# Performance work log

Hardware: AMD Instinct MI355X
Metric: run time of the kernel (lower is better)

The kernel has to match this reference:

```python
import jax, jax.numpy as jnp
import numpy as np

HID = 256   # hidden_dim
P = 16      # pool_size
EPS = 1e-5


def _ln(x, g, b):
    m = x.mean(-1, keepdims=True)
    v = x.var(-1, keepdims=True)
    return (x - m) * jax.lax.rsqrt(v + EPS) * g + b


def setup_inputs() -> dict:
    key = jax.random.key(0)
    ks = jax.random.split(key, 12)
    B, Cf, H, W = 8, 512, 64, 64
    Cg = Cf // 2
    Co = Cf // 2
    s = 0.02
    d = {}
    d['e_f'] = jax.random.normal(ks[0], (B, Cf, H, W), jnp.float32)
    d['e_g'] = jax.random.normal(ks[1], (B, Cg, H, W), jnp.float32)
    d['l_feat'] = jax.random.normal(ks[2], (B, 768, 20), jnp.float32)
    d['l_mask'] = jnp.ones((B, 20, 1), jnp.float32)
    d['ln_f_g'] = jnp.ones((Cf,), jnp.float32)
    d['ln_f_b'] = jnp.zeros((Cf,), jnp.float32)
    d['ln_g_g'] = jnp.ones((Cg,), jnp.float32)
    d['ln_g_b'] = jnp.zeros((Cg,), jnp.float32)
    d['wq'] = jax.random.normal(ks[3], (Cf, HID), jnp.float32) * s
    d['bq'] = jnp.zeros((HID,), jnp.float32)
    d['wk'] = jax.random.normal(ks[4], (Cg, HID), jnp.float32) * s
    d['bk'] = jnp.zeros((HID,), jnp.float32)
    d['wv'] = jax.random.normal(ks[5], (Cg, HID), jnp.float32) * s
    d['bv'] = jnp.zeros((HID,), jnp.float32)
    d['wo'] = jax.random.normal(ks[6], (HID, HID), jnp.float32) * s
    d['bo'] = jnp.zeros((HID,), jnp.float32)
    d['dw_k'] = jax.random.normal(ks[7], (HID, 1, 3, 3), jnp.float32) * s  # depthwise kernel (OIHW, I=1)
    d['efp_w'] = jax.random.normal(ks[8], (HID, Cf), jnp.float32) * s     # 1x1 conv v_channels->hidden
    d['efp_b'] = jnp.zeros((HID,), jnp.float32)
    d['outc_w'] = jax.random.normal(ks[9], (Co, HID), jnp.float32) * s    # 1x1 conv hidden->out
    d['outc_b'] = jnp.zeros((Co,), jnp.float32)
    d['bn_g'] = jnp.ones((Co,), jnp.float32)
    d['bn_b'] = jnp.zeros((Co,), jnp.float32)
    d['bn_m'] = jnp.zeros((Co,), jnp.float32)
    d['bn_v'] = jnp.ones((Co,), jnp.float32)
    return d


def reference(e_f, e_g, l_feat, l_mask, ln_f_g, ln_f_b, ln_g_g, ln_g_b,
              wq, bq, wk, bk, wv, bv, wo, bo, dw_k, efp_w, efp_b,
              outc_w, outc_b, bn_g, bn_b, bn_m, bn_v):
    B, Cf, H, W = e_f.shape
    # Q = w_qi(LN(e_f))                                  (B, HW, HID)
    q = _ln(e_f.transpose(0, 2, 3, 1), ln_f_g, ln_f_b).reshape(B, H * W, Cf) @ wq + bq
    # K/V projections from LN(e_g)
    g = _ln(e_g.transpose(0, 2, 3, 1), ln_g_g, ln_g_b).reshape(B, H * W, -1)
    k = (g @ wk + bk).reshape(B, H, W, HID)
    v = (g @ wv + bv).reshape(B, H, W, HID)
    # 16x16 max/avg pooling -> (B, Hp*Wp, HID)
    k = jnp.max(k.reshape(B, H // P, P, W // P, P, HID), axis=(2, 4)).reshape(B, -1, HID)
    v = jnp.mean(v.reshape(B, H // P, P, W // P, P, HID), axis=(2, 4)).reshape(B, -1, HID)
    # pooled attention
    attn = jax.nn.softmax(jnp.einsum('bqd,bkd->bqk', q, k) * (HID ** -0.5), axis=-1)
    a_i = jnp.einsum('bqk,bkd->bqd', attn, v)  # (B, HW, HID)
    # depthwise 3x3 conv on Q (NCHW)
    q_nchw = q.reshape(B, H, W, HID).transpose(0, 3, 1, 2)
    dw = jax.lax.conv_general_dilated(q_nchw, dw_k, (1, 1), [(1, 1), (1, 1)],
                                      feature_group_count=HID)
    combined = dw + a_i.reshape(B, H, W, HID).transpose(0, 3, 1, 2)
    comb = combined.transpose(0, 2, 3, 1).reshape(B, H * W, HID) @ wo + bo
    comb = comb.reshape(B, H, W, HID).transpose(0, 3, 1, 2)
    # 1x1 proj of e_f, elementwise gate
    efp = jnp.einsum('bchw,oc->bohw', e_f, efp_w) + efp_b[None, :, None, None]
    e_a = efp * comb
    # out: 1x1 conv + BN (inference) + ReLU (dropout inactive in eval)
    out = jnp.einsum('bchw,oc->bohw', e_a, outc_w) + outc_b[None, :, None, None]
    scale = (bn_g * jax.lax.rsqrt(bn_v + EPS))[None, :, None, None]
    out = (out - bn_m[None, :, None, None]) * scale + bn_b[None, :, None, None]
    return jax.nn.relu(out)
```

## Files before the change

kernel.cpp:

```cpp
#include <hip/hip_runtime.h>
#include <math.h>

#define EPS 1e-5f

typedef __attribute__((ext_vector_type(8))) short bf16x8;
typedef __attribute__((ext_vector_type(4))) float f32x4;

__device__ __forceinline__ unsigned short f2bf(float f) {
    unsigned int u = __float_as_uint(f);
    u += 0x7fff + ((u >> 16) & 1);
    return (unsigned short)(u >> 16);
}
__device__ __forceinline__ float bf2f(unsigned short h) {
    return __uint_as_float(((unsigned int)h) << 16);
}
__device__ __forceinline__ float lof(unsigned int u) {
    return __uint_as_float(u << 16);
}
__device__ __forceinline__ float hif(unsigned int u) {
    return __uint_as_float(u & 0xffff0000u);
}
__device__ __forceinline__ void async16(void* lds, const void* g) {
    __builtin_amdgcn_global_load_lds(
        (const __attribute__((address_space(1))) unsigned int*)g,
        (__attribute__((address_space(3))) unsigned int*)lds, 16, 0, 0);
}

__global__ __launch_bounds__(256) void prep_all(
    const float* __restrict__ lnfg, const float* __restrict__ lnfb,
    const float* __restrict__ wq, const float* __restrict__ bq,
    const float* __restrict__ efpw, const float* __restrict__ efpb,
    const float* __restrict__ lngg, const float* __restrict__ lngb,
    const float* __restrict__ wk, const float* __restrict__ bk,
    const float* __restrict__ wv, const float* __restrict__ bv,
    const float* __restrict__ wo, const float* __restrict__ outcw,
    const float* __restrict__ outcb, const float* __restrict__ bng,
    const float* __restrict__ bnb, const float* __restrict__ bnm,
    const float* __restrict__ bnv, const float* __restrict__ dwk,
    unsigned short* __restrict__ Wb1t, unsigned short* __restrict__ Wb2t,
    unsigned short* __restrict__ Wot, unsigned short* __restrict__ Woc,
    float* __restrict__ dwt,
    float* __restrict__ cs1, float* __restrict__ cst1,
    float* __restrict__ cs2, float* __restrict__ cst2,
    float* __restrict__ scv, float* __restrict__ shv)
{
    int idx = blockIdx.x * 256 + threadIdx.x;
    if (idx < 262144) {
        int n = idx >> 9, k = idx & 511;
        float v = (n < 256) ? lnfg[k] * wq[k * 256 + n]
                            : efpw[(size_t)(n - 256) * 512 + k];
        Wb1t[idx] = f2bf(v);
    } else if (idx < 327680) {
        int j = idx - 262144; int n = j >> 8, k = j & 255;
        Wb2t[j] = f2bf(lngg[k] * wk[k * 256 + n]);
    } else if (idx < 393216) {
        int j = idx - 327680; int n = j >> 8, k = j & 255;
        Wot[j] = f2bf(wo[k * 256 + n]);
    } else if (idx < 458752) {
        int j = idx - 393216;
        Woc[j] = f2bf(outcw[j]);
    } else if (idx < 461056) {
        int j = idx - 458752; int tap = j >> 8, ch = j & 255;
        dwt[j] = dwk[ch * 9 + tap];
    } else if (idx < 462336) {
        int j = idx - 461056;
        if (j < 256) {
            int n = j; float cs = 0.f, ct = 0.f;
            for (int k = 0; k < 512; k++) {
                float w = wq[k * 256 + n];
                cs += lnfg[k] * w; ct += lnfb[k] * w;
            }
            cs1[n] = cs; cst1[n] = ct + bq[n];
        } else if (j < 512) {
            cs1[j] = 0.f; cst1[j] = efpb[j - 256];
        } else if (j < 768) {
            int n = j - 512; float cs = 0.f, ct = 0.f;
            for (int k = 0; k < 256; k++) {
                float w = wk[k * 256 + n];
                cs += lngg[k] * w; ct += lngb[k] * w;
            }
            cs2[n] = cs; cst2[n] = ct + bk[n];
        } else if (j < 1024) {
            int n = j - 768; float cs = 0.f, ct = 0.f;
            for (int k = 0; k < 256; k++) {
                float w = wv[k * 256 + n];
                cs += lngg[k] * w; ct += lngb[k] * w;
            }
            cs2[256 + n] = cs; cst2[256 + n] = ct + bv[n];
        } else {
            int n = j - 1024;
            float s = bng[n] * rsqrtf(bnv[n] + EPS);
            scv[n] = s;
            shv[n] = (outcb[n] - bnm[n]) * s + bnb[n];
        }
    }
}

__global__ __launch_bounds__(256) void transpose_fg(
    const float* __restrict__ ef, const float* __restrict__ eg,
    unsigned short* __restrict__ ef_bf, unsigned short* __restrict__ eg_bf,
    float* __restrict__ pf, float* __restrict__ pfq,
    float* __restrict__ pg, float* __restrict__ pgq)
{
    __shared__ float tile[64][65];
    __shared__ float psum[4][64], pss[4][64];
    int id = blockIdx.x;
    const float* src; unsigned short* dst; float* ps; float* pq;
    int C, cblk, b, p0;
    if (id < 2048) {
        src = ef; dst = ef_bf; ps = pf; pq = pfq; C = 512;
        b = id >> 8; cblk = (id >> 5) & 7; p0 = (id & 31) * 128;
    } else {
        id -= 2048;
        src = eg; dst = eg_bf; ps = pg; pq = pgq; C = 256;
        b = id >> 7; cblk = (id >> 5) & 3; p0 = (id & 31) * 128;
    }
    int c0 = cblk * 64;
    const float* s = src + ((size_t)b * C + c0) * 4096 + p0;
    int t = threadIdx.x;
    int cr = t >> 4, p4 = (t & 15) * 4;
    int lane = t & 63, grp = t >> 6;
    int pr = t >> 3, c8 = (t & 7) * 8;

    float4 r1[4], r2[4];
#pragma unroll
    for (int i = 0; i < 4; i++)
        r1[i] = *(const float4*)(s + (size_t)(i * 16 + cr) * 4096 + p4);
#pragma unroll
    for (int i = 0; i < 4; i++)
        r2[i] = *(const float4*)(s + (size_t)(i * 16 + cr) * 4096 + 64 + p4);

#pragma unroll
    for (int half = 0; half < 2; half++) {
#pragma unroll
        for (int i = 0; i < 4; i++) {
            float4 v = half ? r2[i] : r1[i];
            int c = i * 16 + cr;
            tile[c][p4 + 0] = v.x; tile[c][p4 + 1] = v.y;
            tile[c][p4 + 2] = v.z; tile[c][p4 + 3] = v.w;
        }
        __syncthreads();

        int pbase = p0 + half * 64;
        unsigned short* d = dst + ((size_t)(b * 4096 + pbase)) * C + c0;
#pragma unroll
        for (int i = 0; i < 2; i++) {
            int p = i * 32 + pr;
            uint4 pk;
            pk.x = (unsigned)f2bf(tile[c8 + 0][p]) | ((unsigned)f2bf(tile[c8 + 1][p]) << 16);
            pk.y = (unsigned)f2bf(tile[c8 + 2][p]) | ((unsigned)f2bf(tile[c8 + 3][p]) << 16);
            pk.z = (unsigned)f2bf(tile[c8 + 4][p]) | ((unsigned)f2bf(tile[c8 + 5][p]) << 16);
            pk.w = (unsigned)f2bf(tile[c8 + 6][p]) | ((unsigned)f2bf(tile[c8 + 7][p]) << 16);
            *(uint4*)(d + (size_t)p * C + c8) = pk;
        }

        float sm = 0.f, sq = 0.f;
#pragma unroll
        for (int j = 0; j < 16; j++) {
            float v = tile[grp * 16 + j][lane];
            sm += v; sq += v * v;
        }
        psum[grp][lane] = sm; pss[grp][lane] = sq;
        __syncthreads();
        if (t < 64) {
            float fs = psum[0][t] + psum[1][t] + psum[2][t] + psum[3][t];
            float fq = pss[0][t] + pss[1][t] + pss[2][t] + pss[3][t];
            ps[cblk * 32768 + b * 4096 + pbase + t] = fs;
            pq[cblk * 32768 + b * 4096 + pbase + t] = fq;
        }
        if (half == 0) __syncthreads();
    }
}

__global__ __launch_bounds__(256) void ln_finalize(
    const float* __restrict__ pf, const float* __restrict__ pfq,
    const float* __restrict__ pg, const float* __restrict__ pgq,
    float* __restrict__ mf, float* __restrict__ rf,
    float* __restrict__ mg, float* __restrict__ rg)
{
    int gp = blockIdx.x * 256 + threadIdx.x;
    float s = 0.f, q = 0.f;
#pragma unroll
    for (int i = 0; i < 8; i++) { s += pf[i * 32768 + gp]; q += pfq[i * 32768 + gp]; }
    float m = s * (1.f / 512.f);
    float v = q * (1.f / 512.f) - m * m;
    mf[gp] = m; rf[gp] = rsqrtf(v + EPS);
    s = 0.f; q = 0.f;
#pragma unroll
    for (int i = 0; i < 4; i++) { s += pg[i * 32768 + gp]; q += pgq[i * 32768 + gp]; }
    m = s * (1.f / 256.f);
    v = q * (1.f / 256.f) - m * m;
    mg[gp] = m; rg[gp] = rsqrtf(v + EPS);
}

template<int K>
__device__ __forceinline__ void mfma_core(
    const unsigned short* __restrict__ A, const unsigned short* __restrict__ Bt,
    int m0, int n0, unsigned short* As, unsigned short* Bs, f32x4 acc[4][4])
{
    const int tid = threadIdx.x;
    const int wave = tid >> 6, lane = tid & 63;
    const int wm = (wave & 1) * 64, wn = (wave >> 1) * 64;
#pragma unroll
    for (int i = 0; i < 4; i++)
#pragma unroll
        for (int j = 0; j < 4; j++) acc[i][j] = (f32x4){0.f, 0.f, 0.f, 0.f};

    const int srow = wave * 32 + (lane >> 3);
    const int sg = (lane & 7) ^ ((lane >> 3) & 7);
    const unsigned short* ga = A + (size_t)(m0 + srow) * K + sg * 8;
    const unsigned short* gb = Bt + (size_t)(n0 + srow) * K + sg * 8;

    for (int k0 = 0; k0 < K; k0 += 64) {
#pragma unroll
        for (int t = 0; t < 4; t++) {
            async16(As + (wave * 32 + t * 8) * 64, ga + (size_t)t * 8 * K + k0);
            async16(Bs + (wave * 32 + t * 8) * 64, gb + (size_t)t * 8 * K + k0);
        }
        __syncthreads();
#pragma unroll
        for (int ks = 0; ks < 2; ks++) {
            bf16x8 af[4], bfr[4];
            int kb = ks * 4 + (lane >> 4);
            int slot = (kb ^ (lane & 7)) * 8;
#pragma unroll
            for (int i = 0; i < 4; i++) {
                int m = wm + i * 16 + (lane & 15);
                af[i] = *(const bf16x8*)&As[m * 64 + slot];
                int n = wn + i * 16 + (lane & 15);
                bfr[i] = *(const bf16x8*)&Bs[n * 64 + slot];
            }
#pragma unroll
            for (int i = 0; i < 4; i++)
#pragma unroll
                for (int j = 0; j < 4; j++)
                    acc[i][j] = __builtin_amdgcn_mfma_f32_16x16x32_bf16(
                        af[i], bfr[j], acc[i][j], 0, 0, 0);
        }
        __syncthreads();
    }
}

__global__ __launch_bounds__(256, 2) void gemm1_mfma(
    const unsigned short* __restrict__ ef_bf, const unsigned short* __restrict__ Wb1t,
    const float* __restrict__ cs1, const float* __restrict__ cst1,
    const float* __restrict__ mf, const float* __restrict__ rf,
    unsigned short* __restrict__ qbuf, unsigned short* __restrict__ efpbuf)
{
    __shared__ unsigned short As[128 * 64];
    __shared__ unsigned short Bs[256 * 64];
    f32x4 acc[4][8];
    const int tid = threadIdx.x;
    const int wave = tid >> 6, lane = tid & 63;
    const int wm = (wave & 1) * 64, wn = (wave >> 1) * 128;
    const int m0 = blockIdx.x * 128, n0 = blockIdx.y * 256;
#pragma unroll
    for (int i = 0; i < 4; i++)
#pragma unroll
        for (int j = 0; j < 8; j++) acc[i][j] = (f32x4){0.f, 0.f, 0.f, 0.f};

    const int srow = lane >> 3;
    const int sg = (lane & 7) ^ (srow & 7);
    const unsigned short* ga = ef_bf + (size_t)(m0 + wave * 32 + srow) * 512 + sg * 8;
    const unsigned short* gb = Wb1t + (size_t)(n0 + wave * 64 + srow) * 512 + sg * 8;

    for (int k0 = 0; k0 < 512; k0 += 64) {
#pragma unroll
        for (int t = 0; t < 4; t++)
            async16(As + (wave * 32 + t * 8) * 64, ga + (size_t)t * 8 * 512 + k0);
#pragma unroll
        for (int t = 0; t < 8; t++)
            async16(Bs + (wave * 64 + t * 8) * 64, gb + (size_t)t * 8 * 512 + k0);
        __syncthreads();
#pragma unroll
        for (int ks = 0; ks < 2; ks++) {
            bf16x8 af[4], bfr[8];
            int kb = ks * 4 + (lane >> 4);
            int slot = (kb ^ (lane & 7)) * 8;
#pragma unroll
            for (int i = 0; i < 4; i++)
                af[i] = *(const bf16x8*)&As[(wm + i * 16 + (lane & 15)) * 64 + slot];
#pragma unroll
            for (int j = 0; j < 8; j++)
                bfr[j] = *(const bf16x8*)&Bs[(wn + j * 16 + (lane & 15)) * 64 + slot];
#pragma unroll
            for (int i = 0; i < 4; i++)
#pragma unroll
                for (int j = 0; j < 8; j++)
                    acc[i][j] = __builtin_amdgcn_mfma_f32_16x16x32_bf16(
                        af[i], bfr[j], acc[i][j], 0, 0, 0);
        }
        __syncthreads();
    }

    bool isq = (n0 == 0);
#pragma unroll
    for (int i = 0; i < 4; i++) {
#pragma unroll
        for (int r = 0; r < 4; r++) {
            int gm = m0 + wm + i * 16 + ((lane >> 4) * 4) + r;
            float mean = mf[gm], rs = rf[gm];
#pragma unroll
            for (int j = 0; j < 8; j++) {
                int nn = wn + j * 16 + (lane & 15);
                float v = acc[i][j][r];
                if (isq) {
                    int n = nn;
                    float o = rs * (v - mean * cs1[n]) + cst1[n];
                    qbuf[(size_t)gm * 256 + nn] = f2bf(o);
                } else {
                    int n = nn + 256;
                    efpbuf[(size_t)gm * 256 + nn] = f2bf(v + cst1[n]);
                }
            }
        }
    }
}

__global__ __launch_bounds__(256) void gemm2k_mfma(
    const unsigned short* __restrict__ eg_bf, const unsigned short* __restrict__ Wb2t,
    const float* __restrict__ cs2, const float* __restrict__ cst2,
    const float* __restrict__ mg, const float* __restrict__ rg,
    unsigned short* __restrict__ kfull)
{
    __shared__ unsigned short As[8192], Bs[8192];
    f32x4 acc[4][4];
    int m0 = blockIdx.x * 128, n0 = blockIdx.y * 128;
    mfma_core<256>(eg_bf, Wb2t, m0, n0, As, Bs, acc);
    int lane = threadIdx.x & 63, wave = threadIdx.x >> 6;
    int wm = (wave & 1) * 64, wn = (wave >> 1) * 64;
#pragma unroll
    for (int i = 0; i < 4; i++) {
#pragma unroll
        for (int r = 0; r < 4; r++) {
            int gm = m0 + wm + i * 16 + ((lane >> 4) * 4) + r;
            float mean = mg[gm], rs = rg[gm];
#pragma unroll
            for (int j = 0; j < 4; j++) {
                int n = n0 + wn + j * 16 + (lane & 15);
                float o = rs * (acc[i][j][r] - mean * cs2[n]) + cst2[n];
                kfull[(size_t)gm * 256 + n] = f2bf(o);
            }
        }
    }
}

__global__ __launch_bounds__(256) void gemm34_mfma(
    const unsigned short* __restrict__ comb, const unsigned short* __restrict__ Wot,
    const float* __restrict__ bo, const unsigned short* __restrict__ efp,
    const unsigned short* __restrict__ Woc,
    const float* __restrict__ scv, const float* __restrict__ shv,
    float* __restrict__ outp)
{
    __shared__ unsigned short As[64 * 64];
    __shared__ unsigned short Bs[256 * 64];
    __shared__ unsigned short eat[64 * 256];
    const int tid = threadIdx.x;
    const int wave = tid >> 6, lane = tid & 63;
    const int m0 = blockIdx.x * 64;

    const int srow = lane >> 3;
    const int sg = (lane & 7) ^ (srow & 7);

    f32x4 acc[4][4];
#pragma unroll
    for (int i = 0; i < 4; i++)
#pragma unroll
        for (int j = 0; j < 4; j++) acc[i][j] = (f32x4){0.f, 0.f, 0.f, 0.f};

    const unsigned short* ga = comb + (size_t)(m0 + wave * 16 + srow) * 256 + sg * 8;
    const unsigned short* gb = Wot + (size_t)(wave * 64 + srow) * 256 + sg * 8;

    for (int k0 = 0; k0 < 256; k0 += 64) {
#pragma unroll
        for (int t = 0; t < 2; t++)
            async16(As + (wave * 16 + t * 8) * 64, ga + (size_t)t * 8 * 256 + k0);
#pragma unroll
        for (int t = 0; t < 8; t++)
            async16(Bs + (wave * 64 + t * 8) * 64, gb + (size_t)t * 8 * 256 + k0);
        __syncthreads();
#pragma unroll
        for (int ks = 0; ks < 2; ks++) {
            bf16x8 af[4], bfr[4];
            int kb = ks * 4 + (lane >> 4);
            int slot = (kb ^ (lane & 7)) * 8;
#pragma unroll
            for (int i = 0; i < 4; i++) {
                af[i]  = *(const bf16x8*)&As[(i * 16 + (lane & 15)) * 64 + slot];
                bfr[i] = *(const bf16x8*)&Bs[(wave * 64 + i * 16 + (lane & 15)) * 64 + slot];
            }
#pragma unroll
            for (int i = 0; i < 4; i++)
#pragma unroll
                for (int j = 0; j < 4; j++)
                    acc[i][j] = __builtin_amdgcn_mfma_f32_16x16x32_bf16(
                        af[i], bfr[j], acc[i][j], 0, 0, 0);
        }
        __syncthreads();
    }

    float bo4[4];
#pragma unroll
    for (int j = 0; j < 4; j++) bo4[j] = bo[wave * 64 + j * 16 + (lane & 15)];
#pragma unroll
    for (int i = 0; i < 4; i++) {
#pragma unroll
        for (int r = 0; r < 4; r++) {
            int pos = i * 16 + ((lane >> 4) * 4) + r;
#pragma unroll
            for (int j = 0; j < 4; j++) {
                int n = wave * 64 + j * 16 + (lane & 15);
                float o = (acc[i][j][r] + bo4[j])
                          * bf2f(efp[(size_t)(m0 + pos) * 256 + n]);
                int o8 = j * 2 + ((lane >> 3) & 1);
                int slot = o8 ^ (pos & 7);
                eat[pos * 256 + wave * 64 + slot * 8 + (lane & 7)] = f2bf(o);
            }
        }
    }

    f32x4 acc2[4][4];
#pragma unroll
    for (int i = 0; i < 4; i++)
#pragma unroll
        for (int j = 0; j < 4; j++) acc2[i][j] = (f32x4){0.f, 0.f, 0.f, 0.f};

    const unsigned short* gw = Woc + (size_t)(wave * 64 + srow) * 256 + sg * 8;
    for (int k0 = 0; k0 < 256; k0 += 64) {
#pragma unroll
        for (int t = 0; t < 8; t++)
            async16(Bs + (wave * 64 + t * 8) * 64, gw + (size_t)t * 8 * 256 + k0);
        __syncthreads();
        int kc = k0 >> 6;
#pragma unroll
        for (int ks = 0; ks < 2; ks++) {
            bf16x8 af2[4], bf2_[4];
            int kb = ks * 4 + (lane >> 4);
            int slot = (kb ^ (lane & 7)) * 8;
#pragma unroll
            for (int i = 0; i < 4; i++) {
                af2[i]  = *(const bf16x8*)&Bs[(wave * 64 + i * 16 + (lane & 15)) * 64 + slot];
                bf2_[i] = *(const bf16x8*)&eat[(i * 16 + (lane & 15)) * 256 + kc * 64 + slot];
            }
#pragma unroll
            for (int i = 0; i < 4; i++)
#pragma unroll
                for (int j = 0; j < 4; j++)
                    acc2[i][j] = __builtin_amdgcn_mfma_f32_16x16x32_bf16(
                        af2[i], bf2_[j], acc2[i][j], 0, 0, 0);
        }
        __syncthreads();
    }

#pragma unroll
    for (int i = 0; i < 4; i++) {
#pragma unroll
        for (int r = 0; r < 4; r++) {
            int co = wave * 64 + i * 16 + ((lane >> 4) * 4) + r;
            float s = scv[co], hh = shv[co];
#pragma unroll
            for (int j = 0; j < 4; j++) {
                int p = m0 + j * 16 + (lane & 15);
                float o = fmaxf(fmaf(acc2[i][j][r], s, hh), 0.f);
                outp[((size_t)(p >> 12)) * 1048576 + (size_t)co * 4096 + (p & 4095)] = o;
            }
        }
    }
}

__global__ __launch_bounds__(256) void pool_phase(
    const unsigned short* __restrict__ kfull, const float* __restrict__ eg,
    const float* __restrict__ rg, const float* __restrict__ mg,
    unsigned short* __restrict__ kpb, float* __restrict__ s1,
    float* __restrict__ s0)
{
    __shared__ float smem[4352];
    int id = blockIdx.x;
    int t = threadIdx.x;
    if (id < 128) {
        int b = id >> 4, cell = id & 15;
        int hp = cell >> 2, wp = cell & 3;
        int g8 = t & 31, rr = t >> 5;
        float kmx[8];
#pragma unroll
        for (int j = 0; j < 8; j++) kmx[j] = -3.402823466e38f;
#pragma unroll
        for (int rsub = 0; rsub < 2; rsub++) {
            int r = rr * 2 + rsub;
            int prow = (hp * 16 + r) * 64 + wp * 16;
            for (int cl = 0; cl < 16; cl++) {
                size_t basei = ((size_t)(b * 4096 + prow + cl)) * 256 + g8 * 8;
                uint4 kv = *(const uint4*)(kfull + basei);
                kmx[0] = fmaxf(kmx[0], lof(kv.x)); kmx[1] = fmaxf(kmx[1], hif(kv.x));
                kmx[2] = fmaxf(kmx[2], lof(kv.y)); kmx[3] = fmaxf(kmx[3], hif(kv.y));
                kmx[4] = fmaxf(kmx[4], lof(kv.z)); kmx[5] = fmaxf(kmx[5], hif(kv.z));
                kmx[6] = fmaxf(kmx[6], lof(kv.w)); kmx[7] = fmaxf(kmx[7], hif(kv.w));
            }
        }
#pragma unroll
        for (int j = 0; j < 8; j++) smem[rr * 256 + g8 * 8 + j] = kmx[j];
        __syncthreads();
        float m = smem[t];
#pragma unroll
        for (int r2 = 1; r2 < 8; r2++) m = fmaxf(m, smem[r2 * 256 + t]);
        kpb[(size_t)(b * 16 + cell) * 256 + t] = f2bf(m);
    } else {
        int id2 = id - 128;
        int b = id2 >> 6, hp = (id2 >> 4) & 3, cgrp = id2 & 15;
        int rr = t >> 4, cq = t & 15, cx = cq >> 2;
        int p = (hp * 16 + rr) * 64 + cq * 4;
        float4 w4 = *(const float4*)&rg[b * 4096 + p];
        float part[16];
        const float* egb = eg + ((size_t)b * 256 + cgrp * 16) * 4096 + p;
#pragma unroll
        for (int cc = 0; cc < 16; cc++) {
            float4 v4 = *(const float4*)(egb + (size_t)cc * 4096);
            part[cc] = w4.x * v4.x + w4.y * v4.y + w4.z * v4.z + w4.w * v4.w;
        }
#pragma unroll
        for (int cc = 0; cc < 16; cc++) smem[t * 16 + cc] = part[cc];
        if (cgrp == 0) {
            float4 m4 = *(const float4*)&mg[b * 4096 + p];
            smem[4096 + t] = w4.x * m4.x + w4.y * m4.y + w4.z * m4.z + w4.w * m4.w;
        }
        __syncthreads();
        if (t < 64) {
            int cx2 = t >> 4, cc = t & 15;
            float sacc = 0.f;
#pragma unroll
            for (int rr2 = 0; rr2 < 16; rr2++)
#pragma unroll
                for (int dq = 0; dq < 4; dq++)
                    sacc += smem[(rr2 * 16 + cx2 * 4 + dq) * 16 + cc];
            s1[((size_t)(b * 16 + hp * 4 + cx2)) * 256 + cgrp * 16 + cc] = sacc;
        }
        if (cgrp == 0 && t < 4) {
            float sacc = 0.f;
#pragma unroll
            for (int rr2 = 0; rr2 < 16; rr2++)
#pragma unroll
                for (int dq = 0; dq < 4; dq++)
                    sacc += smem[4096 + rr2 * 16 + t * 4 + dq];
            s0[b * 16 + hp * 4 + t] = sacc;
        }
    }
}

__global__ __launch_bounds__(256) void vpool_gemm(
    const float* __restrict__ s1, const float* __restrict__ s0,
    const float* __restrict__ lngg, const float* __restrict__ wv,
    const float* __restrict__ cs2, const float* __restrict__ cst2,
    float* __restrict__ vp)
{
    int cell = blockIdx.x;
    int n = threadIdx.x;
    const float* s1r = s1 + (size_t)cell * 256;
    float acc = 0.f;
    for (int c = 0; c < 256; c++)
        acc = fmaf(lngg[c] * s1r[c], wv[c * 256 + n], acc);
    vp[(size_t)cell * 256 + n] = acc * (1.f / 256.f)
        - (s0[cell] * (1.f / 256.f)) * cs2[256 + n] + cst2[256 + n];
}

__global__ __launch_bounds__(256) void combined_dw(
    const unsigned short* __restrict__ qbuf, const unsigned short* __restrict__ kpb,
    const float* __restrict__ vp, const float* __restrict__ dwt,
    unsigned short* __restrict__ combined)
{
    __shared__ float attns[256];
    int wave = threadIdx.x >> 6, lane = threadIdx.x & 63;
    int id = blockIdx.x;
    int b = id & 7, seg = id >> 3;
    int pidx0 = seg * 16;

    if (wave == 0) {
        int fr = lane & 15, quad = lane >> 4;
        const unsigned short* qrow = qbuf + (size_t)(b * 4096 + pidx0 + fr) * 256 + quad * 8;
        const unsigned short* krow = kpb + (size_t)(b * 16 + fr) * 256 + quad * 8;
        f32x4 sacc = {0.f, 0.f, 0.f, 0.f};
#pragma unroll
        for (int ks = 0; ks < 8; ks++) {
            bf16x8 af = *(const bf16x8*)(qrow + ks * 32);
            bf16x8 bf_ = *(const bf16x8*)(krow + ks * 32);
            sacc = __builtin_amdgcn_mfma_f32_16x16x32_bf16(af, bf_, sacc, 0, 0, 0);
        }
#pragma unroll
        for (int r = 0; r < 4; r++) {
            float s = sacc[r] * 0.0625f;
            float mx = s;
#pragma unroll
            for (int off = 8; off >= 1; off >>= 1) mx = fmaxf(mx, __shfl_xor(mx, off));
            float e = __expf(s - mx);
            float sum = e;
#pragma unroll
            for (int off = 8; off >= 1; off >>= 1) sum += __shfl_xor(sum, off);
            attns[(quad * 4 + r) * 16 + fr] = e / sum;
        }
    }
    __syncthreads();

    int pidx = pidx0 + wave * 4;
    int h = pidx >> 6, w0 = pidx & 63;
    int o4 = lane * 4;

    float4 kreg[9];
#pragma unroll
    for (int tap = 0; tap < 9; tap++)
        kreg[tap] = *(const float4*)&dwt[tap * 256 + o4];

    float4 acc[4];
#pragma unroll
    for (int i = 0; i < 4; i++) acc[i] = (float4){0.f, 0.f, 0.f, 0.f};

    const float* arow = attns + (wave * 4) * 16;
#pragma unroll
    for (int c = 0; c < 16; c++) {
        float4 v = *(const float4*)&vp[(size_t)(b * 16 + c) * 256 + o4];
#pragma unroll
        for (int i = 0; i < 4; i++) {
            float a = arow[i * 16 + c];
            acc[i].x = fmaf(a, v.x, acc[i].x); acc[i].y = fmaf(a, v.y, acc[i].y);
            acc[i].z = fmaf(a, v.z, acc[i].z); acc[i].w = fmaf(a, v.w, acc[i].w);
        }
    }
#pragma unroll
    for (int dy = 0; dy < 3; dy++) {
        int hh = h + dy - 1;
        if (hh < 0 || hh > 63) continue;
        const unsigned short* qr = qbuf + ((size_t)(b * 4096 + hh * 64)) * 256;
        float4 ft[6];
#pragma unroll
        for (int c = 0; c < 6; c++) {
            int xx = w0 - 1 + c;
            if (xx < 0 || xx > 63) {
                ft[c] = (float4){0.f, 0.f, 0.f, 0.f};
            } else {
                uint2 qa = *(const uint2*)(qr + (size_t)xx * 256 + o4);
                ft[c] = (float4){lof(qa.x), hif(qa.x), lof(qa.y), hif(qa.y)};
            }
        }
#pragma unroll
        for (int dx = 0; dx < 3; dx++) {
            float4 kk = kreg[dy * 3 + dx];
#pragma unroll
            for (int i = 0; i < 4; i++) {
                float4 qv = ft[i + dx];
                acc[i].x = fmaf(qv.x, kk.x, acc[i].x);
                acc[i].y = fmaf(qv.y, kk.y, acc[i].y);
                acc[i].z = fmaf(qv.z, kk.z, acc[i].z);
                acc[i].w = fmaf(qv.w, kk.w, acc[i].w);
            }
        }
    }
#pragma unroll
    for (int i = 0; i < 4; i++) {
        uint2 pk;
        pk.x = (unsigned)f2bf(acc[i].x) | ((unsigned)f2bf(acc[i].y) << 16);
        pk.y = (unsigned)f2bf(acc[i].z) | ((unsigned)f2bf(acc[i].w) << 16);
        *(uint2*)(combined + ((size_t)(b * 4096 + pidx + i)) * 256 + o4) = pk;
    }
}

extern "C" void kernel_launch(void* const* d_in, const int* in_sizes, int n_in,
                              void* d_out, int out_size, void* d_ws, size_t ws_size,
                              hipStream_t stream)
{
    const float* e_f   = (const float*)d_in[0];
    const float* e_g   = (const float*)d_in[1];
    const float* lnfg  = (const float*)d_in[4];
    const float* lnfb  = (const float*)d_in[5];
    const float* lngg  = (const float*)d_in[6];
    const float* lngb  = (const float*)d_in[7];
    const float* wq    = (const float*)d_in[8];
    const float* bq    = (const float*)d_in[9];
    const float* wk    = (const float*)d_in[10];
    const float* bk    = (const float*)d_in[11];
    const float* wv    = (const float*)d_in[12];
    const float* bv    = (const float*)d_in[13];
    const float* wo    = (const float*)d_in[14];
    const float* bo    = (const float*)d_in[15];
    const float* dwk   = (const float*)d_in[16];
    const float* efpw  = (const float*)d_in[17];
    const float* efpb  = (const float*)d_in[18];
    const float* outcw = (const float*)d_in[19];
    const float* outcb = (const float*)d_in[20];
    const float* bng   = (const float*)d_in[21];
    const float* bnb   = (const float*)d_in[22];
    const float* bnm   = (const float*)d_in[23];
    const float* bnv   = (const float*)d_in[24];
    float* outp = (float*)d_out;

    char* base = (char*)d_ws;
    auto alloc = [&](size_t bytes) -> char* {
        char* r = base; base += (bytes + 255) & ~(size_t)255; return r;
    };
    float* pf    = (float*)alloc(8 * 32768 * 4);
    float* pfq   = (float*)alloc(8 * 32768 * 4);
    float* pg    = (float*)alloc(4 * 32768 * 4);
    float* pgq   = (float*)alloc(4 * 32768 * 4);
    float* mf    = (float*)alloc(32768 * 4);
    float* rf    = (float*)alloc(32768 * 4);
    float* mg    = (float*)alloc(32768 * 4);
    float* rg    = (float*)alloc(32768 * 4);
    float* cs1   = (float*)alloc(512 * 4);
    float* cst1  = (float*)alloc(512 * 4);
    float* cs2   = (float*)alloc(512 * 4);
    float* cst2  = (float*)alloc(512 * 4);
    float* scv   = (float*)alloc(256 * 4);
    float* shv   = (float*)alloc(256 * 4);
    float* dwt   = (float*)alloc(9 * 256 * 4);
    unsigned short* Wb1t = (unsigned short*)alloc(262144 * 2);
    unsigned short* Wb2t = (unsigned short*)alloc(65536 * 2);
    unsigned short* Wot  = (unsigned short*)alloc(65536 * 2);
    unsigned short* Woc  = (unsigned short*)alloc(65536 * 2);
    unsigned short* ef_bf = (unsigned short*)alloc((size_t)32768 * 512 * 2);
    unsigned short* eg_bf = (unsigned short*)alloc((size_t)32768 * 256 * 2);
    unsigned short* qbuf  = (unsigned short*)alloc((size_t)32768 * 256 * 2);
    unsigned short* efpbuf = (unsigned short*)alloc((size_t)32768 * 256 * 2);
    unsigned short* kfull = (unsigned short*)alloc((size_t)32768 * 256 * 2);
    unsigned short* kpb  = (unsigned short*)alloc(128 * 256 * 2);
    float* vp    = (float*)alloc(128 * 256 * 4);
    float* s1    = (float*)alloc(128 * 256 * 4);
    float* s0    = (float*)alloc(128 * 4);

    prep_all<<<1806, 256, 0, stream>>>(
        lnfg, lnfb, wq, bq, efpw, efpb, lngg, lngb, wk, bk, wv, bv, wo,
        outcw, outcb, bng, bnb, bnm, bnv, dwk,
        Wb1t, Wb2t, Wot, Woc, dwt, cs1, cst1, cs2, cst2, scv, shv);
    transpose_fg<<<3072, 256, 0, stream>>>(e_f, e_g, ef_bf, eg_bf,
                                           pf, pfq, pg, pgq);
    ln_finalize<<<128, 256, 0, stream>>>(pf, pfq, pg, pgq, mf, rf, mg, rg);
    gemm1_mfma<<<dim3(256, 2), 256, 0, stream>>>(ef_bf, Wb1t, cs1, cst1, mf, rf,
                                                 qbuf, efpbuf);
    gemm2k_mfma<<<dim3(256, 2), 256, 0, stream>>>(eg_bf, Wb2t, cs2, cst2, mg, rg,
                                                  kfull);
    pool_phase<<<640, 256, 0, stream>>>(kfull, e_g, rg, mg, kpb, s1, s0);
    vpool_gemm<<<128, 256, 0, stream>>>(s1, s0, lngg, wv, cs2, cst2, vp);
    combined_dw<<<2048, 256, 0, stream>>>(qbuf, kpb, vp, dwt, kfull);
    gemm34_mfma<<<512, 256, 0, stream>>>(kfull, Wot, bo, efpbuf,
                                         Woc, scv, shv, outp);
}
```

Before: 316.7 us.

## Fuse LN finalize into GEMMs and attention/depthwise into output GEMM kernel

Removes the ln_finalize kernel by having each GEMM block reduce the partial LayerNorm sums for its own rows into shared memory, with gemm2k also writing the e_g stats needed later. It also merges combined_dw into the output GEMM kernel, so the combined attention plus depthwise tile is built straight in LDS and never round-trips through global memory. The aim is fewer launches and less global traffic for the combined buffer. In exchange the fused kernel has a larger LDS footprint (comb, Bs, attns), which may lower occupancy, and each block redundantly re-reads q neighbours for the depthwise conv.

```diff
diff --git a/kernel.cpp b/kernel.cpp
--- a/kernel.cpp
+++ b/kernel.cpp
@@ -172,88 +172,31 @@
     }
 }
 
-__global__ __launch_bounds__(256) void ln_finalize(
-    const float* __restrict__ pf, const float* __restrict__ pfq,
-    const float* __restrict__ pg, const float* __restrict__ pgq,
-    float* __restrict__ mf, float* __restrict__ rf,
-    float* __restrict__ mg, float* __restrict__ rg)
-{
-    int gp = blockIdx.x * 256 + threadIdx.x;
-    float s = 0.f, q = 0.f;
-#pragma unroll
-    for (int i = 0; i < 8; i++) { s += pf[i * 32768 + gp]; q += pfq[i * 32768 + gp]; }
-    float m = s * (1.f / 512.f);
-    float v = q * (1.f / 512.f) - m * m;
-    mf[gp] = m; rf[gp] = rsqrtf(v + EPS);
-    s = 0.f; q = 0.f;
-#pragma unroll
-    for (int i = 0; i < 4; i++) { s += pg[i * 32768 + gp]; q += pgq[i * 32768 + gp]; }
-    m = s * (1.f / 256.f);
-    v = q * (1.f / 256.f) - m * m;
-    mg[gp] = m; rg[gp] = rsqrtf(v + EPS);
-}
-
-template<int K>
-__device__ __forceinline__ void mfma_core(
-    const unsigned short* __restrict__ A, const unsigned short* __restrict__ Bt,
-    int m0, int n0, unsigned short* As, unsigned short* Bs, f32x4 acc[4][4])
-{
-    const int tid = threadIdx.x;
-    const int wave = tid >> 6, lane = tid & 63;
-    const int wm = (wave & 1) * 64, wn = (wave >> 1) * 64;
-#pragma unroll
-    for (int i = 0; i < 4; i++)
-#pragma unroll
-        for (int j = 0; j < 4; j++) acc[i][j] = (f32x4){0.f, 0.f, 0.f, 0.f};
-
-    const int srow = wave * 32 + (lane >> 3);
-    const int sg = (lane & 7) ^ ((lane >> 3) & 7);
-    const unsigned short* ga = A + (size_t)(m0 + srow) * K + sg * 8;
-    const unsigned short* gb = Bt + (size_t)(n0 + srow) * K + sg * 8;
-
-    for (int k0 = 0; k0 < K; k0 += 64) {
-#pragma unroll
-        for (int t = 0; t < 4; t++) {
-            async16(As + (wave * 32 + t * 8) * 64, ga + (size_t)t * 8 * K + k0);
-            async16(Bs + (wave * 32 + t * 8) * 64, gb + (size_t)t * 8 * K + k0);
-        }
-        __syncthreads();
-#pragma unroll
-        for (int ks = 0; ks < 2; ks++) {
-            bf16x8 af[4], bfr[4];
-            int kb = ks * 4 + (lane >> 4);
-            int slot = (kb ^ (lane & 7)) * 8;
-#pragma unroll
-            for (int i = 0; i < 4; i++) {
-                int m = wm + i * 16 + (lane & 15);
-                af[i] = *(const bf16x8*)&As[m * 64 + slot];
-                int n = wn + i * 16 + (lane & 15);
-                bfr[i] = *(const bf16x8*)&Bs[n * 64 + slot];
-            }
-#pragma unroll
-            for (int i = 0; i < 4; i++)
-#pragma unroll
-                for (int j = 0; j < 4; j++)
-                    acc[i][j] = __builtin_amdgcn_mfma_f32_16x16x32_bf16(
-                        af[i], bfr[j], acc[i][j], 0, 0, 0);
-        }
-        __syncthreads();
-    }
-}
-
 __global__ __launch_bounds__(256, 2) void gemm1_mfma(
     const unsigned short* __restrict__ ef_bf, const unsigned short* __restrict__ Wb1t,
     const float* __restrict__ cs1, const float* __restrict__ cst1,
-    const float* __restrict__ mf, const float* __restrict__ rf,
+    const float* __restrict__ pf, const float* __restrict__ pfq,
     unsigned short* __restrict__ qbuf, unsigned short* __restrict__ efpbuf)
 {
     __shared__ unsigned short As[128 * 64];
     __shared__ unsigned short Bs[256 * 64];
+    __shared__ float smf[128], srf[128];
     f32x4 acc[4][8];
     const int tid = threadIdx.x;
     const int wave = tid >> 6, lane = tid & 63;
     const int wm = (wave & 1) * 64, wn = (wave >> 1) * 128;
     const int m0 = blockIdx.x * 128, n0 = blockIdx.y * 256;
+
+    if (tid < 128) {
+        int gm = m0 + tid;
+        float s = 0.f, q = 0.f;
+#pragma unroll
+        for (int i = 0; i < 8; i++) { s += pf[i * 32768 + gm]; q += pfq[i * 32768 + gm]; }
+        float m = s * (1.f / 512.f);
+        smf[tid] = m;
+        srf[tid] = rsqrtf(q * (1.f / 512.f) - m * m + EPS);
+    }
+
 #pragma unroll
     for (int i = 0; i < 4; i++)
 #pragma unroll
@@ -298,8 +241,9 @@
     for (int i = 0; i < 4; i++) {
 #pragma unroll
         for (int r = 0; r < 4; r++) {
-            int gm = m0 + wm + i * 16 + ((lane >> 4) * 4) + r;
-            float mean = mf[gm], rs = rf[gm];
+            int lm = wm + i * 16 + ((lane >> 4) * 4) + r;
+            int gm = m0 + lm;
+            float mean = smf[lm], rs = srf[lm];
 #pragma unroll
             for (int j = 0; j < 8; j++) {
                 int nn = wn + j * 16 + (lane & 15);
@@ -317,152 +261,93 @@
     }
 }
 
+template<int K>
+__device__ __forceinline__ void mfma_core(
+    const unsigned short* __restrict__ A, const unsigned short* __restrict__ Bt,
+    int m0, int n0, unsigned short* As, unsigned short* Bs, f32x4 acc[4][4])
+{
+    const int tid = threadIdx.x;
+    const int wave = tid >> 6, lane = tid & 63;
+    const int wm = (wave & 1) * 64, wn = (wave >> 1) * 64;
+#pragma unroll
+    for (int i = 0; i < 4; i++)
+#pragma unroll
+        for (int j = 0; j < 4; j++) acc[i][j] = (f32x4){0.f, 0.f, 0.f, 0.f};
+
+    const int srow = wave * 32 + (lane >> 3);
+    const int sg = (lane & 7) ^ ((lane >> 3) & 7);
+    const unsigned short* ga = A + (size_t)(m0 + srow) * K + sg * 8;
+    const unsigned short* gb = Bt + (size_t)(n0 + srow) * K + sg * 8;
+
+    for (int k0 = 0; k0 < K; k0 += 64) {
+#pragma unroll
+        for (int t = 0; t < 4; t++) {
+            async16(As + (wave * 32 + t * 8) * 64, ga + (size_t)t * 8 * K + k0);
+            async16(Bs + (wave * 32 + t * 8) * 64, gb + (size_t)t * 8 * K + k0);
+        }
+        __syncthreads();
+#pragma unroll
+        for (int ks = 0; ks < 2; ks++) {
+            bf16x8 af[4], bfr[4];
+            int kb = ks * 4 + (lane >> 4);
+            int slot = (kb ^ (lane & 7)) * 8;
+#pragma unroll
+            for (int i = 0; i < 4; i++) {
+                int m = wm + i * 16 + (lane & 15);
+                af[i] = *(const bf16x8*)&As[m * 64 + slot];
+                int n = wn + i * 16 + (lane & 15);
+                bfr[i] = *(const bf16x8*)&Bs[n * 64 + slot];
+            }
+#pragma unroll
+            for (int i = 0; i < 4; i++)
+#pragma unroll
+                for (int j = 0; j < 4; j++)
+                    acc[i][j] = __builtin_amdgcn_mfma_f32_16x16x32_bf16(
+                        af[i], bfr[j], acc[i][j], 0, 0, 0);
+        }
+        __syncthreads();
+    }
+}
+
 __global__ __launch_bounds__(256) void gemm2k_mfma(
     const unsigned short* __restrict__ eg_bf, const unsigned short* __restrict__ Wb2t,
     const float* __restrict__ cs2, const float* __restrict__ cst2,
-    const float* __restrict__ mg, const float* __restrict__ rg,
+    const float* __restrict__ pg, const float* __restrict__ pgq,
+    float* __restrict__ mg, float* __restrict__ rg,
     unsigned short* __restrict__ kfull)
 {
     __shared__ unsigned short As[8192], Bs[8192];
+    __shared__ float smg[128], srg[128];
     f32x4 acc[4][4];
     int m0 = blockIdx.x * 128, n0 = blockIdx.y * 128;
+    int tid = threadIdx.x;
+
+    if (tid < 128) {
+        int gm = m0 + tid;
+        float s = 0.f, q = 0.f;
+#pragma unroll
+        for (int i = 0; i < 4; i++) { s += pg[i * 32768 + gm]; q += pgq[i * 32768 + gm]; }
+        float m = s * (1.f / 256.f);
+        float r = rsqrtf(q * (1.f / 256.f) - m * m + EPS);
+        smg[tid] = m; srg[tid] = r;
+        if (n0 == 0) { mg[gm] = m; rg[gm] = r; }
+    }
+
     mfma_core<256>(eg_bf, Wb2t, m0, n0, As, Bs, acc);
-    int lane = threadIdx.x & 63, wave = threadIdx.x >> 6;
+    int lane = tid & 63, wave = tid >> 6;
     int wm = (wave & 1) * 64, wn = (wave >> 1) * 64;
 #pragma unroll
     for (int i = 0; i < 4; i++) {
 #pragma unroll
         for (int r = 0; r < 4; r++) {
-            int gm = m0 + wm + i * 16 + ((lane >> 4) * 4) + r;
-            float mean = mg[gm], rs = rg[gm];
+            int lm = wm + i * 16 + ((lane >> 4) * 4) + r;
+            int gm = m0 + lm;
+            float mean = smg[lm], rs = srg[lm];
 #pragma unroll
             for (int j = 0; j < 4; j++) {
                 int n = n0 + wn + j * 16 + (lane & 15);
                 float o = rs * (acc[i][j][r] - mean * cs2[n]) + cst2[n];
                 kfull[(size_t)gm * 256 + n] = f2bf(o);
-            }
-        }
-    }
-}
-
-__global__ __launch_bounds__(256) void gemm34_mfma(
-    const unsigned short* __restrict__ comb, const unsigned short* __restrict__ Wot,
-    const float* __restrict__ bo, const unsigned short* __restrict__ efp,
-    const unsigned short* __restrict__ Woc,
-    const float* __restrict__ scv, const float* __restrict__ shv,
-    float* __restrict__ outp)
-{
-    __shared__ unsigned short As[64 * 64];
-    __shared__ unsigned short Bs[256 * 64];
-    __shared__ unsigned short eat[64 * 256];
-    const int tid = threadIdx.x;
-    const int wave = tid >> 6, lane = tid & 63;
-    const int m0 = blockIdx.x * 64;
-
-    const int srow = lane >> 3;
-    const int sg = (lane & 7) ^ (srow & 7);
-
-    f32x4 acc[4][4];
-#pragma unroll
-    for (int i = 0; i < 4; i++)
-#pragma unroll
-        for (int j = 0; j < 4; j++) acc[i][j] = (f32x4){0.f, 0.f, 0.f, 0.f};
-
-    const unsigned short* ga = comb + (size_t)(m0 + wave * 16 + srow) * 256 + sg * 8;
-    const unsigned short* gb = Wot + (size_t)(wave * 64 + srow) * 256 + sg * 8;
-
-    for (int k0 = 0; k0 < 256; k0 += 64) {
-#pragma unroll
-        for (int t = 0; t < 2; t++)
-            async16(As + (wave * 16 + t * 8) * 64, ga + (size_t)t * 8 * 256 + k0);
-#pragma unroll
-        for (int t = 0; t < 8; t++)
-            async16(Bs + (wave * 64 + t * 8) * 64, gb + (size_t)t * 8 * 256 + k0);
-        __syncthreads();
-#pragma unroll
-        for (int ks = 0; ks < 2; ks++) {
-            bf16x8 af[4], bfr[4];
-            int kb = ks * 4 + (lane >> 4);
-            int slot = (kb ^ (lane & 7)) * 8;
-#pragma unroll
-            for (int i = 0; i < 4; i++) {
-                af[i]  = *(const bf16x8*)&As[(i * 16 + (lane & 15)) * 64 + slot];
-                bfr[i] = *(const bf16x8*)&Bs[(wave * 64 + i * 16 + (lane & 15)) * 64 + slot];
-            }
-#pragma unroll
-            for (int i = 0; i < 4; i++)
-#pragma unroll
-                for (int j = 0; j < 4; j++)
-                    acc[i][j] = __builtin_amdgcn_mfma_f32_16x16x32_bf16(
-                        af[i], bfr[j], acc[i][j], 0, 0, 0);
-        }
-        __syncthreads();
-    }
-
-    float bo4[4];
-#pragma unroll
-    for (int j = 0; j < 4; j++) bo4[j] = bo[wave * 64 + j * 16 + (lane & 15)];
-#pragma unroll
-    for (int i = 0; i < 4; i++) {
-#pragma unroll
-        for (int r = 0; r < 4; r++) {
-            int pos = i * 16 + ((lane >> 4) * 4) + r;
-#pragma unroll
-            for (int j = 0; j < 4; j++) {
-                int n = wave * 64 + j * 16 + (lane & 15);
-                float o = (acc[i][j][r] + bo4[j])
-                          * bf2f(efp[(size_t)(m0 + pos) * 256 + n]);
-                int o8 = j * 2 + ((lane >> 3) & 1);
-                int slot = o8 ^ (pos & 7);
-                eat[pos * 256 + wave * 64 + slot * 8 + (lane & 7)] = f2bf(o);
-            }
-        }
-    }
-
-    f32x4 acc2[4][4];
-#pragma unroll
-    for (int i = 0; i < 4; i++)
-#pragma unroll
-        for (int j = 0; j < 4; j++) acc2[i][j] = (f32x4){0.f, 0.f, 0.f, 0.f};
-
-    const unsigned short* gw = Woc + (size_t)(wave * 64 + srow) * 256 + sg * 8;
-    for (int k0 = 0; k0 < 256; k0 += 64) {
-#pragma unroll
-        for (int t = 0; t < 8; t++)
-            async16(Bs + (wave * 64 + t * 8) * 64, gw + (size_t)t * 8 * 256 + k0);
-        __syncthreads();
-        int kc = k0 >> 6;
-#pragma unroll
-        for (int ks = 0; ks < 2; ks++) {
-            bf16x8 af2[4], bf2_[4];
-            int kb = ks * 4 + (lane >> 4);
-            int slot = (kb ^ (lane & 7)) * 8;
-#pragma unroll
-            for (int i = 0; i < 4; i++) {
-                af2[i]  = *(const bf16x8*)&Bs[(wave * 64 + i * 16 + (lane & 15)) * 64 + slot];
-                bf2_[i] = *(const bf16x8*)&eat[(i * 16 + (lane & 15)) * 256 + kc * 64 + slot];
-            }
-#pragma unroll
-            for (int i = 0; i < 4; i++)
-#pragma unroll
-                for (int j = 0; j < 4; j++)
-                    acc2[i][j] = __builtin_amdgcn_mfma_f32_16x16x32_bf16(
-                        af2[i], bf2_[j], acc2[i][j], 0, 0, 0);
-        }
-        __syncthreads();
-    }
-
-#pragma unroll
-    for (int i = 0; i < 4; i++) {
-#pragma unroll
-        for (int r = 0; r < 4; r++) {
-            int co = wave * 64 + i * 16 + ((lane >> 4) * 4) + r;
-            float s = scv[co], hh = shv[co];
-#pragma unroll
-            for (int j = 0; j < 4; j++) {
-                int p = m0 + j * 16 + (lane & 15);
-                float o = fmaxf(fmaf(acc2[i][j][r], s, hh), 0.f);
-                outp[((size_t)(p >> 12)) * 1048576 + (size_t)co * 4096 + (p & 4095)] = o;
             }
         }
     }
@@ -562,20 +447,28 @@
         - (s0[cell] * (1.f / 256.f)) * cs2[256 + n] + cst2[256 + n];
 }
 
-__global__ __launch_bounds__(256) void combined_dw(
+__global__ __launch_bounds__(256) void fused_cdw34(
     const unsigned short* __restrict__ qbuf, const unsigned short* __restrict__ kpb,
     const float* __restrict__ vp, const float* __restrict__ dwt,
-    unsigned short* __restrict__ combined)
-{
-    __shared__ float attns[256];
-    int wave = threadIdx.x >> 6, lane = threadIdx.x & 63;
-    int id = blockIdx.x;
-    int b = id & 7, seg = id >> 3;
-    int pidx0 = seg * 16;
-
-    if (wave == 0) {
+    const unsigned short* __restrict__ Wot, const float* __restrict__ bo,
+    const unsigned short* __restrict__ efp, const unsigned short* __restrict__ Woc,
+    const float* __restrict__ scv, const float* __restrict__ shv,
+    float* __restrict__ outp)
+{
+    __shared__ unsigned short comb[64 * 256];
+    __shared__ unsigned short Bs[256 * 64];
+    __shared__ float attns[1024];
+    const int tid = threadIdx.x;
+    const int wave = tid >> 6, lane = tid & 63;
+    const int m0 = blockIdx.x * 64;
+    const int b = m0 >> 12;
+    const int prow0 = m0 & 4095;
+    const int h = prow0 >> 6;
+
+    {
         int fr = lane & 15, quad = lane >> 4;
-        const unsigned short* qrow = qbuf + (size_t)(b * 4096 + pidx0 + fr) * 256 + quad * 8;
+        const unsigned short* qrow =
+            qbuf + (size_t)(b * 4096 + prow0 + wave * 16 + fr) * 256 + quad * 8;
         const unsigned short* krow = kpb + (size_t)(b * 16 + fr) * 256 + quad * 8;
         f32x4 sacc = {0.f, 0.f, 0.f, 0.f};
 #pragma unroll
@@ -594,70 +487,181 @@
             float sum = e;
 #pragma unroll
             for (int off = 8; off >= 1; off >>= 1) sum += __shfl_xor(sum, off);
-            attns[(quad * 4 + r) * 16 + fr] = e / sum;
+            attns[wave * 256 + (quad * 4 + r) * 16 + fr] = e / sum;
+        }
+    }
+
+    {
+        int o4 = lane * 4;
+        float4 kreg[9];
+#pragma unroll
+        for (int tap = 0; tap < 9; tap++)
+            kreg[tap] = *(const float4*)&dwt[tap * 256 + o4];
+        const float* arow_base = attns + wave * 256;
+        const int kcq = lane >> 4;
+        const int kbq = (lane >> 1) & 7;
+        const int koff = (lane & 1) * 4;
+
+#pragma unroll
+        for (int sub = 0; sub < 4; sub++) {
+            int p0w = wave * 16 + sub * 4;
+            float4 acc[4];
+#pragma unroll
+            for (int i = 0; i < 4; i++) acc[i] = (float4){0.f, 0.f, 0.f, 0.f};
+#pragma unroll
+            for (int c = 0; c < 16; c++) {
+                float4 v = *(const float4*)&vp[(size_t)(b * 16 + c) * 256 + o4];
+#pragma unroll
+                for (int i = 0; i < 4; i++) {
+                    float a = arow_base[(sub * 4 + i) * 16 + c];
+                    acc[i].x = fmaf(a, v.x, acc[i].x); acc[i].y = fmaf(a, v.y, acc[i].y);
+                    acc[i].z = fmaf(a, v.z, acc[i].z); acc[i].w = fmaf(a, v.w, acc[i].w);
+                }
+            }
+#pragma unroll
+            for (int dy = 0; dy < 3; dy++) {
+                int hh = h + dy - 1;
+                if (hh < 0 || hh > 63) continue;
+                const unsigned short* qr = qbuf + ((size_t)(b * 4096 + hh * 64)) * 256;
+                float4 ft[6];
+#pragma unroll
+                for (int c = 0; c < 6; c++) {
+                    int xx = p0w - 1 + c;
+                    if (xx < 0 || xx > 63) {
+                        ft[c] = (float4){0.f, 0.f, 0.f, 0.f};
+                    } else {
+                        uint2 qa = *(const uint2*)(qr + (size_t)xx * 256 + o4);
+                        ft[c] = (float4){lof(qa.x), hif(qa.x), lof(qa.y), hif(qa.y)};
+                    }
+                }
+#pragma unroll
+                for (int dx = 0; dx < 3; dx++) {
+                    float4 kk = kreg[dy * 3 + dx];
+#pragma unroll
+                    for (int i = 0; i < 4; i++) {
+                        float4 qv = ft[i + dx];
+                        acc[i].x = fmaf(qv.x, kk.x, acc[i].x);
+                        acc[i].y = fmaf(qv.y, kk.y, acc[i].y);
+                        acc[i].z = fmaf(qv.z, kk.z, acc[i].z);
+                        acc[i].w = fmaf(qv.w, kk.w, acc[i].w);
+                    }
+                }
+            }
+#pragma unroll
+            for (int i = 0; i < 4; i++) {
+                int p = p0w + i;
+                uint2 pk;
+                pk.x = (unsigned)f2bf(acc[i].x) | ((unsigned)f2bf(acc[i].y) << 16);
+                pk.y = (unsigned)f2bf(acc[i].z) | ((unsigned)f2bf(acc[i].w) << 16);
+                *(uint2*)&comb[p * 256 + kcq * 64 + (kbq ^ (p & 7)) * 8 + koff] = pk;
+            }
         }
     }
     __syncthreads();
 
-    int pidx = pidx0 + wave * 4;
-    int h = pidx >> 6, w0 = pidx & 63;
-    int o4 = lane * 4;
-
-    float4 kreg[9];
-#pragma unroll
-    for (int tap = 0; tap < 9; tap++)
-        kreg[tap] = *(const float4*)&dwt[tap * 256 + o4];
-
-    float4 acc[4];
-#pragma unroll
-    for (int i = 0; i < 4; i++) acc[i] = (float4){0.f, 0.f, 0.f, 0.f};
-
-    const float* arow = attns + (wave * 4) * 16;
-#pragma unroll
-    for (int c = 0; c < 16; c++) {
-        float4 v = *(const float4*)&vp[(size_t)(b * 16 + c) * 256 + o4];
-#pragma unroll
-        for (int i = 0; i < 4; i++) {
-            float a = arow[i * 16 + c];
-            acc[i].x = fmaf(a, v.x, acc[i].x); acc[i].y = fmaf(a, v.y, acc[i].y);
-            acc[i].z = fmaf(a, v.z, acc[i].z); acc[i].w = fmaf(a, v.w, acc[i].w);
-        }
-    }
-#pragma unroll
-    for (int dy = 0; dy < 3; dy++) {
-        int hh = h + dy - 1;
-        if (hh < 0 || hh > 63) continue;
-        const unsigned short* qr = qbuf + ((size_t)(b * 4096 + hh * 64)) * 256;
-        float4 ft[6];
-#pragma unroll
-        for (int c = 0; c < 6; c++) {
-            int xx = w0 - 1 + c;
-            if (xx < 0 || xx > 63) {
-                ft[c] = (float4){0.f, 0.f, 0.f, 0.f};
-            } else {
-                uint2 qa = *(const uint2*)(qr + (size_t)xx * 256 + o4);
-                ft[c] = (float4){lof(qa.x), hif(qa.x), lof(qa.y), hif(qa.y)};
-            }
-        }
-#pragma unroll
-        for (int dx = 0; dx < 3; dx++) {
-            float4 kk = kreg[dy * 3 + dx];
+    const int srow = lane >> 3;
+    const int sg = (lane & 7) ^ (srow & 7);
+
+    f32x4 acc[4][4];
+#pragma unroll
+    for (int i = 0; i < 4; i++)
+#pragma unroll
+        for (int j = 0; j < 4; j++) acc[i][j] = (f32x4){0.f, 0.f, 0.f, 0.f};
+
+    const unsigned short* gb = Wot + (size_t)(wave * 64 + srow) * 256 + sg * 8;
+    for (int k0 = 0; k0 < 256; k0 += 64) {
+#pragma unroll
+        for (int t = 0; t < 8; t++)
+            async16(Bs + (wave * 64 + t * 8) * 64, gb + (size_t)t * 8 * 256 + k0);
+        __syncthreads();
+        int kc = k0 >> 6;
+#pragma unroll
+        for (int ks = 0; ks < 2; ks++) {
+            bf16x8 af[4], bfr[4];
+            int kb = ks * 4 + (lane >> 4);
+            int slot = (kb ^ (lane & 7)) * 8;
 #pragma unroll
             for (int i = 0; i < 4; i++) {
-                float4 qv = ft[i + dx];
-                acc[i].x = fmaf(qv.x, kk.x, acc[i].x);
-                acc[i].y = fmaf(qv.y, kk.y, acc[i].y);
-                acc[i].z = fmaf(qv.z, kk.z, acc[i].z);
-                acc[i].w = fmaf(qv.w, kk.w, acc[i].w);
-            }
-        }
-    }
+                af[i]  = *(const bf16x8*)&comb[(i * 16 + (lane & 15)) * 256 + kc * 64 + slot];
+                bfr[i] = *(const bf16x8*)&Bs[(wave * 64 + i * 16 + (lane & 15)) * 64 + slot];
+            }
+#pragma unroll
+            for (int i = 0; i < 4; i++)
+#pragma unroll
+                for (int j = 0; j < 4; j++)
+                    acc[i][j] = __builtin_amdgcn_mfma_f32_16x16x32_bf16(
+                        af[i], bfr[j], acc[i][j], 0, 0, 0);
+        }
+        __syncthreads();
+    }
+    unsigned short* eat = comb;
+
+    float bo4[4];
+#pragma unroll
+    for (int j = 0; j < 4; j++) bo4[j] = bo[wave * 64 + j * 16 + (lane & 15)];
 #pragma unroll
     for (int i = 0; i < 4; i++) {
-        uint2 pk;
-        pk.x = (unsigned)f2bf(acc[i].x) | ((unsigned)f2bf(acc[i].y) << 16);
-        pk.y = (unsigned)f2bf(acc[i].z) | ((unsigned)f2bf(acc[i].w) << 16);
-        *(uint2*)(combined + ((size_t)(b * 4096 + pidx + i)) * 256 + o4) = pk;
+#pragma unroll
+        for (int r = 0; r < 4; r++) {
+            int pos = i * 16 + ((lane >> 4) * 4) + r;
+#pragma unroll
+            for (int j = 0; j < 4; j++) {
+                int n = wave * 64 + j * 16 + (lane & 15);
+                float o = (acc[i][j][r] + bo4[j])
+                          * bf2f(efp[(size_t)(m0 + pos) * 256 + n]);
+                int o8 = j * 2 + ((lane >> 3) & 1);
+                int slot = o8 ^ (pos & 7);
+                eat[pos * 256 + wave * 64 + slot * 8 + (lane & 7)] = f2bf(o);
+            }
+        }
+    }
+
+    f32x4 acc2[4][4];
+#pragma unroll
+    for (int i = 0; i < 4; i++)
+#pragma unroll
+        for (int j = 0; j < 4; j++) acc2[i][j] = (f32x4){0.f, 0.f, 0.f, 0.f};
+
+    const unsigned short* gw = Woc + (size_t)(wave * 64 + srow) * 256 + sg * 8;
+    for (int k0 = 0; k0 < 256; k0 += 64) {
+#pragma unroll
+        for (int t = 0; t < 8; t++)
+            async16(Bs + (wave * 64 + t * 8) * 64, gw + (size_t)t * 8 * 256 + k0);
+        __syncthreads();
+        int kc = k0 >> 6;
+#pragma unroll
+        for (int ks = 0; ks < 2; ks++) {
+            bf16x8 af2[4], bf2_[4];
+            int kb = ks * 4 + (lane >> 4);
+            int slot = (kb ^ (lane & 7)) * 8;
+#pragma unroll
+            for (int i = 0; i < 4; i++) {
+                af2[i]  = *(const bf16x8*)&Bs[(wave * 64 + i * 16 + (lane & 15)) * 64 + slot];
+                bf2_[i] = *(const bf16x8*)&eat[(i * 16 + (lane & 15)) * 256 + kc * 64 + slot];
+            }
+#pragma unroll
+            for (int i = 0; i < 4; i++)
+#pragma unroll
+                for (int j = 0; j < 4; j++)
+                    acc2[i][j] = __builtin_amdgcn_mfma_f32_16x16x32_bf16(
+                        af2[i], bf2_[j], acc2[i][j], 0, 0, 0);
+        }
+        __syncthreads();
+    }
+
+#pragma unroll
+    for (int i = 0; i < 4; i++) {
+#pragma unroll
+        for (int r = 0; r < 4; r++) {
+            int co = wave * 64 + i * 16 + ((lane >> 4) * 4) + r;
+            float s = scv[co], hh2 = shv[co];
+#pragma unroll
+            for (int j = 0; j < 4; j++) {
+                int p = m0 + j * 16 + (lane & 15);
+                float o = fmaxf(fmaf(acc2[i][j][r], s, hh2), 0.f);
+                outp[((size_t)(p >> 12)) * 1048576 + (size_t)co * 4096 + (p & 4095)] = o;
+            }
+        }
     }
 }
 
@@ -698,8 +702,6 @@
     float* pfq   = (float*)alloc(8 * 32768 * 4);
     float* pg    = (float*)alloc(4 * 32768 * 4);
     float* pgq   = (float*)alloc(4 * 32768 * 4);
-    float* mf    = (float*)alloc(32768 * 4);
-    float* rf    = (float*)alloc(32768 * 4);
     float* mg    = (float*)alloc(32768 * 4);
     float* rg    = (float*)alloc(32768 * 4);
     float* cs1   = (float*)alloc(512 * 4);
@@ -729,14 +731,12 @@
         Wb1t, Wb2t, Wot, Woc, dwt, cs1, cst1, cs2, cst2, scv, shv);
     transpose_fg<<<3072, 256, 0, stream>>>(e_f, e_g, ef_bf, eg_bf,
                                            pf, pfq, pg, pgq);
-    ln_finalize<<<128, 256, 0, stream>>>(pf, pfq, pg, pgq, mf, rf, mg, rg);
-    gemm1_mfma<<<dim3(256, 2), 256, 0, stream>>>(ef_bf, Wb1t, cs1, cst1, mf, rf,
+    gemm1_mfma<<<dim3(256, 2), 256, 0, stream>>>(ef_bf, Wb1t, cs1, cst1, pf, pfq,
                                                  qbuf, efpbuf);
-    gemm2k_mfma<<<dim3(256, 2), 256, 0, stream>>>(eg_bf, Wb2t, cs2, cst2, mg, rg,
-                                                  kfull);
+    gemm2k_mfma<<<dim3(256, 2), 256, 0, stream>>>(eg_bf, Wb2t, cs2, cst2, pg, pgq,
+                                                  mg, rg, kfull);
     pool_phase<<<640, 256, 0, stream>>>(kfull, e_g, rg, mg, kpb, s1, s0);
     vpool_gemm<<<128, 256, 0, stream>>>(s1, s0, lngg, wv, cs2, cst2, vp);
-    combined_dw<<<2048, 256, 0, stream>>>(qbuf, kpb, vp, dwt, kfull);
-    gemm34_mfma<<<512, 256, 0, stream>>>(kfull, Wot, bo, efpbuf,
+    fused_cdw34<<<512, 256, 0, stream>>>(qbuf, kpb, vp, dwt, Wot, bo, efpbuf,
                                          Woc, scv, shv, outp);
 }
```

Measured after the change: 370.6 us. 17.0% more time.
